# Performance work log

Hardware: AMD Instinct MI355X
Metric: run time of the kernel (lower is better)

## Reference

```python
import jax, jax.numpy as jnp
import numpy as np

N_ATOMS = 20
LS_PER_ATOM = [0, 0, 1, 1, 2]   # two s, two p, one d shell per atom
N_PRIM = 8
N_COORDS = 131072


def cart_angulars(l):
    return np.array([[lx, ly, l - lx - ly]
                     for lx in range(l, -1, -1)
                     for ly in range(l - lx, -1, -1)], dtype=np.float32)


def fact2(n):
    n = int(n)
    if n <= 0:
        return 1.0
    r = 1.0
    while n > 1:
        r *= n
        n -= 2
    return r


# ---- static shell bookkeeping (grouped by angular momentum l) ----
SHELL_ATOM = np.array([a for a in range(N_ATOMS) for _ in LS_PER_ATOM])
SHELL_L = np.array([l for _ in range(N_ATOMS) for l in LS_PER_ATOM])
N_SHELLS = len(SHELL_L)
UNIQUE_LS = sorted(set(LS_PER_ATOM))

GROUPS = {}
for l in UNIQUE_LS:
    idx = np.where(SHELL_L == l)[0]
    ls = cart_angulars(l)  # [ncart, 3]
    anorms = 1.0 / np.sqrt(np.array(
        [np.prod([fact2(2 * int(e) - 1) for e in row]) for row in ls],
        dtype=np.float64))
    GROUPS[l] = (idx, ls, anorms.astype(np.float32))

NAO_CART = sum(len(GROUPS[l][1]) * len(GROUPS[l][0]) for l in UNIQUE_LS)  # 280
NAO_SPH = sum((2 * l + 1) * len(GROUPS[l][0]) for l in UNIQUE_LS)          # 260


def setup_inputs() -> dict:
    key = jax.random.key(0)
    k1, k2, k3, k4, k5, k6 = jax.random.split(key, 6)
    coords = jax.random.normal(k1, (N_COORDS, 3), dtype=jnp.float32) * 2.0
    centers = jax.random.normal(k2, (N_ATOMS, 3), dtype=jnp.float32) * 3.0
    # Gaussian exponents must be positive
    zetas = jax.random.uniform(k3, (N_SHELLS, N_PRIM), dtype=jnp.float32,
                               minval=0.2, maxval=3.0)
    coeffs = jax.random.normal(k4, (N_SHELLS, N_PRIM), dtype=jnp.float32)
    normalization = jax.random.uniform(k5, (NAO_CART,), dtype=jnp.float32,
                                       minval=0.5, maxval=1.5)
    cart2sph = jax.random.normal(k6, (NAO_CART, NAO_SPH), dtype=jnp.float32) * 0.3
    return {"coords": coords, "centers": centers, "zetas": zetas,
            "coeffs": coeffs, "normalization": normalization,
            "cart2sph": cart2sph}


def reference(coords, centers, zetas, coeffs, normalization, cart2sph):
    """Batched GTOBasis.eval_ao: [N,3] -> [N, nao_sph]."""
    n = coords.shape[0]
    pieces = []
    for l in UNIQUE_LS:
        idx, ls, anorms = GROUPS[l]
        c = centers[SHELL_ATOM[idx]]                 # [S, 3]
        rs = coords[:, None, :] - c[None]            # [N, S, 3]
        rs2 = jnp.sum(rs * rs, axis=-1)              # [N, S]
        # cartesian angular part: prod over xyz of rs**l_component
        ang = jnp.prod(rs[:, :, None, :] ** jnp.asarray(ls)[None, None],
                       axis=-1)                      # [N, S, ncart]
        ex = jnp.exp(-zetas[idx][None] * rs2[:, :, None])  # [N, S, nprim]
        rad = jnp.sum(coeffs[idx][None] * ex, axis=-1)     # [N, S]
        phis = jnp.asarray(anorms) * ang * rad[:, :, None]  # [N, S, ncart]
        pieces.append(phis.reshape(n, -1))
    aos = jnp.concatenate(pieces, axis=-1) * normalization  # [N, nao_cart]
    return jnp.dot(aos, cart2sph)                           # [N, nao_sph]
```

## Files before the change

kernel.cpp:

```cpp
#include <hip/hip_runtime.h>

typedef unsigned int uint;
typedef unsigned short ushort;
typedef __attribute__((ext_vector_type(8))) short short8;
typedef __attribute__((ext_vector_type(4))) float f32x4;

#define NSH   100
#define NPRIM 8
#define NAOC  280
#define NAOS  260
#define NATOM 20
#define KP    288
#define NKB   9
#define MT    32
#define NTHR  256
#define NCOLP 272
#define BCH   (32 * NCOLP)
#define RSQRT3 0.57735026918962576f
#define LOG2E  1.4426950408889634f
#define EPS   276

#define O_AH    0
#define O_AL    18432
#define O_ZETA  36864
#define O_COEF  40064
#define O_CEN   43264
#define O_CX    43584
#define O_CY    43712
#define O_CZ    43840
#define POOLSZ  43968

__device__ __forceinline__ ushort bf16_rne(float x) {
    uint u = __float_as_uint(x);
    return (ushort)((u + 0x7FFFu + ((u >> 16) & 1u)) >> 16);
}
__device__ __forceinline__ float bf16_to_f(ushort h) {
    return __uint_as_float(((uint)h) << 16);
}
__device__ __forceinline__ uint cvt_pk_bf16(float a, float b) {
    uint r;
    asm("v_cvt_pk_bf16_f32 %0, %1, %2" : "=v"(r) : "v"(a), "v"(b));
    return r;
}

__device__ __forceinline__ float b_src(const float* __restrict__ c2s,
                                       const float* __restrict__ norm,
                                       int kp, int col) {
    if (kp >= NAOC || col >= NAOS) return 0.0f;
    int a = kp / 14, i = kp - 14 * a;
    int ksrc; float an = 1.0f;
    if (i < 2)      ksrc = 2 * a + i;
    else if (i < 8) ksrc = 40 + 6 * a + (i - 2);
    else {
        ksrc = 160 + 6 * a + (i - 8);
        if (i == 8 || i == 11 || i == 13) an = RSQRT3;
    }
    return c2s[ksrc * NAOS + col] * norm[ksrc] * an;
}

__global__ void prep_b(const float* __restrict__ c2s, const float* __restrict__ norm,
                       ushort* __restrict__ wsHi, ushort* __restrict__ wsLo) {
    int id = blockIdx.x * 256 + threadIdx.x;
    if (id >= KP * NCOLP) return;
    int k = id / NCOLP, col = id % NCOLP;
    float v = b_src(c2s, norm, k, col);
    ushort hi = bf16_rne(v);
    ushort lo = bf16_rne(v - bf16_to_f(hi));
    int off = (k >> 5) * BCH +
              (((col >> 4) * 4 + ((k & 31) >> 3)) * 16 + (col & 15)) * 8 + (k & 7);
    wsHi[off] = hi;
    wsLo[off] = lo;
}

template <bool USEWS>
__global__ __launch_bounds__(NTHR, 4) void gto_mfma(
    const float* __restrict__ coords, const float* __restrict__ centers,
    const float* __restrict__ zetas, const float* __restrict__ coeffs,
    const float* __restrict__ norm, const float* __restrict__ c2s,
    const ushort* __restrict__ wsHi, const ushort* __restrict__ wsLo,
    float* __restrict__ out, int n)
{
    __shared__ __align__(16) char smem[POOLSZ];
    float*  sZeta = (float*)(smem + O_ZETA);
    float*  sCoef = (float*)(smem + O_COEF);
    float4* sCen4 = (float4*)(smem + O_CEN);
    float*  sCx   = (float*)(smem + O_CX);
    float*  sCy   = (float*)(smem + O_CY);
    float*  sCz   = (float*)(smem + O_CZ);

    const int t = threadIdx.x, lane = t & 63, w = t >> 6;
    const int lr = lane & 15, lg4 = lane >> 4;
    const int P0 = blockIdx.x * MT;

    for (int i = t; i < NSH * NPRIM; i += NTHR) {
        sZeta[i] = zetas[i] * LOG2E;
        sCoef[i] = coeffs[i];
    }
    if (t < NATOM)
        sCen4[t] = make_float4(centers[3 * t], centers[3 * t + 1], centers[3 * t + 2], 0.0f);
    if (t < MT * 3) {
        int gi = P0 * 3 + t;
        float v = (gi < 3 * n) ? coords[gi] : 0.0f;
        int p = t / 3, c = t - 3 * (t / 3);
        if (c == 0) sCx[p] = v; else if (c == 1) sCy[p] = v; else sCz[p] = v;
    }
    if (t < 64)        *(uint2*)(smem + O_AH + 35 * 512 + t * 8) = make_uint2(0u, 0u);
    else if (t < 128)  *(uint2*)(smem + O_AL + 35 * 512 + (t - 64) * 8) = make_uint2(0u, 0u);
    __syncthreads();

    const int pA = t & 31, ag = t >> 5;
    const float cxp = sCx[pA], cyp = sCy[pA], czp = sCz[pA];

    auto doAtom = [&](int a) {
        float4 ca = sCen4[a];
        float dx = cxp - ca.x, dy = cyp - ca.y, dz = czp - ca.z;
        float r2 = dx * dx + dy * dy + dz * dz;
        float rad[5];
        #pragma unroll
        for (int sh = 0; sh < 5; ++sh) {
            const float* z = &sZeta[(5 * a + sh) * NPRIM];
            const float* cf = &sCoef[(5 * a + sh) * NPRIM];
            float4 z0 = *(const float4*)z,  z1 = *(const float4*)(z + 4);
            float4 c0 = *(const float4*)cf, c1 = *(const float4*)(cf + 4);
            float r = c0.x * __builtin_amdgcn_exp2f(-z0.x * r2);
            r += c0.y * __builtin_amdgcn_exp2f(-z0.y * r2);
            r += c0.z * __builtin_amdgcn_exp2f(-z0.z * r2);
            r += c0.w * __builtin_amdgcn_exp2f(-z0.w * r2);
            r += c1.x * __builtin_amdgcn_exp2f(-z1.x * r2);
            r += c1.y * __builtin_amdgcn_exp2f(-z1.y * r2);
            r += c1.z * __builtin_amdgcn_exp2f(-z1.z * r2);
            r += c1.w * __builtin_amdgcn_exp2f(-z1.w * r2);
            rad[sh] = r;
        }
        float xx = dx * dx, xy = dx * dy, xz = dx * dz;
        float yy = dy * dy, yz = dy * dz, zz = dz * dz;
        float v[14] = { rad[0], rad[1],
                        dx * rad[2], dy * rad[2], dz * rad[2],
                        dx * rad[3], dy * rad[3], dz * rad[3],
                        xx * rad[4], xy * rad[4], xz * rad[4],
                        yy * rad[4], yz * rad[4], zz * rad[4] };
        const int k0 = a * 14;
        #pragma unroll
        for (int pr = 0; pr < 7; ++pr) {
            int k = k0 + 2 * pr;
            uint h = cvt_pk_bf16(v[2 * pr], v[2 * pr + 1]);
            float r0 = v[2 * pr]     - __uint_as_float(h << 16);
            float r1 = v[2 * pr + 1] - __uint_as_float(h & 0xffff0000u);
            uint l = cvt_pk_bf16(r0, r1);
            const int off = (k >> 3) * 512 + pA * 16 + (k & 7) * 2;
            *(uint*)(smem + O_AH + off) = h;
            *(uint*)(smem + O_AL + off) = l;
        }
    };
    if (ag < 4) { doAtom(3 * ag); doAtom(3 * ag + 1); doAtom(3 * ag + 2); }
    else        { int b = 12 + 2 * (ag - 4); doAtom(b); doAtom(b + 1); }
    __syncthreads();

    const ushort* pH  = wsHi + (4 * w * 64 + lane) * 8;
    const ushort* pL  = wsLo + (4 * w * 64 + lane) * 8;
    const ushort* pH2 = wsHi + (16 * 64 + lane) * 8;
    const ushort* pL2 = wsLo + (16 * 64 + lane) * 8;

    f32x4 acc[5][2];
    #pragma unroll
    for (int i = 0; i < 5; ++i)
        #pragma unroll
        for (int mt = 0; mt < 2; ++mt)
            acc[i][mt] = (f32x4){0.0f, 0.0f, 0.0f, 0.0f};

    #pragma unroll 1
    for (int kb = 0; kb < NKB; ++kb) {
        short8 aH[2], aL[2];
        #pragma unroll
        for (int mt = 0; mt < 2; ++mt) {
            const int off = (kb * 4 + lg4) * 512 + (mt * 16 + lr) * 16;
            aH[mt] = *(const short8*)(smem + O_AH + off);
            aL[mt] = *(const short8*)(smem + O_AL + off);
        }
        #pragma unroll
        for (int i = 0; i < 5; ++i) {
            if (i < 4 || w == 0) {
                short8 bh, bl;
                if (USEWS) {
                    if (i < 4) { bh = *(const short8*)(pH + i * 512);
                                 bl = *(const short8*)(pL + i * 512); }
                    else       { bh = *(const short8*)pH2;
                                 bl = *(const short8*)pL2; }
                } else {
                    int nt = (i == 4) ? 16 : (4 * w + i);
                    #pragma unroll
                    for (int j = 0; j < 8; ++j) {
                        int k = kb * 32 + lg4 * 8 + j;
                        int col = nt * 16 + lr;
                        float v = b_src(c2s, norm, k, col);
                        ushort hi = bf16_rne(v);
                        bh[j] = (short)hi;
                        bl[j] = (short)bf16_rne(v - bf16_to_f(hi));
                    }
                }
                #pragma unroll
                for (int mt = 0; mt < 2; ++mt)
                    acc[i][mt] = __builtin_amdgcn_mfma_f32_16x16x32_bf16(aH[mt], bh, acc[i][mt], 0, 0, 0);
                #pragma unroll
                for (int mt = 0; mt < 2; ++mt)
                    acc[i][mt] = __builtin_amdgcn_mfma_f32_16x16x32_bf16(aH[mt], bl, acc[i][mt], 0, 0, 0);
                #pragma unroll
                for (int mt = 0; mt < 2; ++mt)
                    acc[i][mt] = __builtin_amdgcn_mfma_f32_16x16x32_bf16(aL[mt], bh, acc[i][mt], 0, 0, 0);
            }
        }
        pH += BCH; pL += BCH; pH2 += BCH; pL2 += BCH;
    }

    float* ep = (float*)smem;
    #pragma unroll
    for (int mt = 0; mt < 2; ++mt) {
        __syncthreads();
        #pragma unroll
        for (int i = 0; i < 5; ++i) {
            if (i < 4 || w == 0) {
                int nt = (i == 4) ? 16 : (4 * w + i);
                int col = nt * 16 + lr;
                #pragma unroll
                for (int r = 0; r < 4; ++r)
                    ep[(lg4 * 4 + r) * EPS + col] = acc[i][mt][r];
            }
        }
        __syncthreads();
        #pragma unroll
        for (int j = 0; j < 4; ++j) {
            int row = w + j * 4;
            int P = P0 + mt * 16 + row;
            if (P < n)
                *(float4*)&out[(size_t)P * NAOS + lane * 4] = *(const float4*)&ep[row * EPS + lane * 4];
        }
        if (w == 1 && lane < 16) {
            int P = P0 + mt * 16 + lane;
            if (P < n)
                *(float4*)&out[(size_t)P * NAOS + 256] = *(const float4*)&ep[lane * EPS + 256];
        }
    }
}

extern "C" void kernel_launch(void* const* d_in, const int* in_sizes, int n_in,
                              void* d_out, int out_size, void* d_ws, size_t ws_size,
                              hipStream_t stream) {
    const float* coords  = (const float*)d_in[0];
    const float* centers = (const float*)d_in[1];
    const float* zetas   = (const float*)d_in[2];
    const float* coeffs  = (const float*)d_in[3];
    const float* norm    = (const float*)d_in[4];
    const float* c2s     = (const float*)d_in[5];
    float* out = (float*)d_out;
    int n = in_sizes[0] / 3;
    int grid = (n + MT - 1) / MT;

    ushort* wsHi = (ushort*)d_ws;
    ushort* wsLo = wsHi + (size_t)KP * NCOLP;
    const size_t WS_NEED = (size_t)2 * KP * NCOLP * sizeof(ushort);

    if (ws_size >= WS_NEED) {
        prep_b<<<(KP * NCOLP + 255) / 256, 256, 0, stream>>>(c2s, norm, wsHi, wsLo);
        gto_mfma<true><<<grid, NTHR, 0, stream>>>(coords, centers, zetas, coeffs, norm, c2s,
                                                  wsHi, wsLo, out, n);
    } else {
        gto_mfma<false><<<grid, NTHR, 0, stream>>>(coords, centers, zetas, coeffs, norm, c2s,
                                                   nullptr, nullptr, out, n);
    }
}
```

Measured before the change: 91.88 us.

## Pad K to 16 per atom, vectorize A stores, hoist B loads, single epilogue

Repacks the K dimension so each atom occupies 16 slots (14 used, 2 zero), letting each atom's bf16 hi/lo values go to shared memory as 128-bit stores instead of many 32-bit stores, and drops the separate zero-fill of the padding. B fragments for all five N-tiles are loaded at the top of each K step so the global loads overlap instead of sitting between MFMAs. The epilogue writes both M-subtiles to shared memory in one pass with one barrier pair. The cost is an extra K block (10 instead of 9) of MFMA work, more shared memory, and occupancy lowered to 3 blocks per SM in the launch bounds.

```diff
diff --git a/kernel.cpp b/kernel.cpp
--- a/kernel.cpp
+++ b/kernel.cpp
@@ -10,8 +10,8 @@
 #define NAOC  280
 #define NAOS  260
 #define NATOM 20
-#define KP    288
-#define NKB   9
+#define KP    320
+#define NKB   10
 #define MT    32
 #define NTHR  256
 #define NCOLP 272
@@ -21,14 +21,14 @@
 #define EPS   276
 
 #define O_AH    0
-#define O_AL    18432
-#define O_ZETA  36864
-#define O_COEF  40064
-#define O_CEN   43264
-#define O_CX    43584
-#define O_CY    43712
-#define O_CZ    43840
-#define POOLSZ  43968
+#define O_AL    20480
+#define O_ZETA  40960
+#define O_COEF  44160
+#define O_CEN   47360
+#define O_CX    47680
+#define O_CY    47808
+#define O_CZ    47936
+#define POOLSZ  48064
 
 __device__ __forceinline__ ushort bf16_rne(float x) {
     uint u = __float_as_uint(x);
@@ -46,8 +46,9 @@
 __device__ __forceinline__ float b_src(const float* __restrict__ c2s,
                                        const float* __restrict__ norm,
                                        int kp, int col) {
-    if (kp >= NAOC || col >= NAOS) return 0.0f;
-    int a = kp / 14, i = kp - 14 * a;
+    if (kp >= KP || col >= NAOS) return 0.0f;
+    int a = kp >> 4, i = kp & 15;
+    if (i >= 14) return 0.0f;
     int ksrc; float an = 1.0f;
     if (i < 2)      ksrc = 2 * a + i;
     else if (i < 8) ksrc = 40 + 6 * a + (i - 2);
@@ -73,7 +74,7 @@
 }
 
 template <bool USEWS>
-__global__ __launch_bounds__(NTHR, 4) void gto_mfma(
+__global__ __launch_bounds__(NTHR, 3) void gto_mfma(
     const float* __restrict__ coords, const float* __restrict__ centers,
     const float* __restrict__ zetas, const float* __restrict__ coeffs,
     const float* __restrict__ norm, const float* __restrict__ c2s,
@@ -104,8 +105,6 @@
         int p = t / 3, c = t - 3 * (t / 3);
         if (c == 0) sCx[p] = v; else if (c == 1) sCy[p] = v; else sCz[p] = v;
     }
-    if (t < 64)        *(uint2*)(smem + O_AH + 35 * 512 + t * 8) = make_uint2(0u, 0u);
-    else if (t < 128)  *(uint2*)(smem + O_AL + 35 * 512 + (t - 64) * 8) = make_uint2(0u, 0u);
     __syncthreads();
 
     const int pA = t & 31, ag = t >> 5;
@@ -139,18 +138,19 @@
                         dx * rad[3], dy * rad[3], dz * rad[3],
                         xx * rad[4], xy * rad[4], xz * rad[4],
                         yy * rad[4], yz * rad[4], zz * rad[4] };
-        const int k0 = a * 14;
+        uint h[7], l[7];
         #pragma unroll
         for (int pr = 0; pr < 7; ++pr) {
-            int k = k0 + 2 * pr;
-            uint h = cvt_pk_bf16(v[2 * pr], v[2 * pr + 1]);
-            float r0 = v[2 * pr]     - __uint_as_float(h << 16);
-            float r1 = v[2 * pr + 1] - __uint_as_float(h & 0xffff0000u);
-            uint l = cvt_pk_bf16(r0, r1);
-            const int off = (k >> 3) * 512 + pA * 16 + (k & 7) * 2;
-            *(uint*)(smem + O_AH + off) = h;
-            *(uint*)(smem + O_AL + off) = l;
-        }
+            h[pr] = cvt_pk_bf16(v[2 * pr], v[2 * pr + 1]);
+            float r0 = v[2 * pr]     - __uint_as_float(h[pr] << 16);
+            float r1 = v[2 * pr + 1] - __uint_as_float(h[pr] & 0xffff0000u);
+            l[pr] = cvt_pk_bf16(r0, r1);
+        }
+        const int off = a * 1024 + pA * 16;
+        *(uint4*)(smem + O_AH + off)       = make_uint4(h[0], h[1], h[2], h[3]);
+        *(uint4*)(smem + O_AH + off + 512) = make_uint4(h[4], h[5], h[6], 0u);
+        *(uint4*)(smem + O_AL + off)       = make_uint4(l[0], l[1], l[2], l[3]);
+        *(uint4*)(smem + O_AL + off + 512) = make_uint4(l[4], l[5], l[6], 0u);
     };
     if (ag < 4) { doAtom(3 * ag); doAtom(3 * ag + 1); doAtom(3 * ag + 2); }
     else        { int b = 12 + 2 * (ag - 4); doAtom(b); doAtom(b + 1); }
@@ -170,6 +170,33 @@
 
     #pragma unroll 1
     for (int kb = 0; kb < NKB; ++kb) {
+        short8 bh[5], bl[5];
+        if (USEWS) {
+            #pragma unroll
+            for (int i = 0; i < 4; ++i) {
+                bh[i] = *(const short8*)(pH + i * 512);
+                bl[i] = *(const short8*)(pL + i * 512);
+            }
+            if (w == 0) {
+                bh[4] = *(const short8*)pH2;
+                bl[4] = *(const short8*)pL2;
+            }
+        } else {
+            #pragma unroll
+            for (int i = 0; i < 5; ++i) {
+                int nt = (i == 4) ? 16 : (4 * w + i);
+                #pragma unroll
+                for (int j = 0; j < 8; ++j) {
+                    int k = kb * 32 + lg4 * 8 + j;
+                    int col = nt * 16 + lr;
+                    float v = b_src(c2s, norm, k, col);
+                    ushort hi = bf16_rne(v);
+                    bh[i][j] = (short)hi;
+                    bl[i][j] = (short)bf16_rne(v - bf16_to_f(hi));
+                }
+            }
+        }
+
         short8 aH[2], aL[2];
         #pragma unroll
         for (int mt = 0; mt < 2; ++mt) {
@@ -177,68 +204,51 @@
             aH[mt] = *(const short8*)(smem + O_AH + off);
             aL[mt] = *(const short8*)(smem + O_AL + off);
         }
+
         #pragma unroll
         for (int i = 0; i < 5; ++i) {
             if (i < 4 || w == 0) {
-                short8 bh, bl;
-                if (USEWS) {
-                    if (i < 4) { bh = *(const short8*)(pH + i * 512);
-                                 bl = *(const short8*)(pL + i * 512); }
-                    else       { bh = *(const short8*)pH2;
-                                 bl = *(const short8*)pL2; }
-                } else {
-                    int nt = (i == 4) ? 16 : (4 * w + i);
-                    #pragma unroll
-                    for (int j = 0; j < 8; ++j) {
-                        int k = kb * 32 + lg4 * 8 + j;
-                        int col = nt * 16 + lr;
-                        float v = b_src(c2s, norm, k, col);
-                        ushort hi = bf16_rne(v);
-                        bh[j] = (short)hi;
-                        bl[j] = (short)bf16_rne(v - bf16_to_f(hi));
-                    }
-                }
                 #pragma unroll
                 for (int mt = 0; mt < 2; ++mt)
-                    acc[i][mt] = __builtin_amdgcn_mfma_f32_16x16x32_bf16(aH[mt], bh, acc[i][mt], 0, 0, 0);
+                    acc[i][mt] = __builtin_amdgcn_mfma_f32_16x16x32_bf16(aH[mt], bh[i], acc[i][mt], 0, 0, 0);
                 #pragma unroll
                 for (int mt = 0; mt < 2; ++mt)
-                    acc[i][mt] = __builtin_amdgcn_mfma_f32_16x16x32_bf16(aH[mt], bl, acc[i][mt], 0, 0, 0);
+                    acc[i][mt] = __builtin_amdgcn_mfma_f32_16x16x32_bf16(aH[mt], bl[i], acc[i][mt], 0, 0, 0);
                 #pragma unroll
                 for (int mt = 0; mt < 2; ++mt)
-                    acc[i][mt] = __builtin_amdgcn_mfma_f32_16x16x32_bf16(aL[mt], bh, acc[i][mt], 0, 0, 0);
+                    acc[i][mt] = __builtin_amdgcn_mfma_f32_16x16x32_bf16(aL[mt], bh[i], acc[i][mt], 0, 0, 0);
             }
         }
         pH += BCH; pL += BCH; pH2 += BCH; pL2 += BCH;
     }
 
+    __syncthreads();
     float* ep = (float*)smem;
     #pragma unroll
-    for (int mt = 0; mt < 2; ++mt) {
-        __syncthreads();
-        #pragma unroll
-        for (int i = 0; i < 5; ++i) {
-            if (i < 4 || w == 0) {
-                int nt = (i == 4) ? 16 : (4 * w + i);
-                int col = nt * 16 + lr;
+    for (int i = 0; i < 5; ++i) {
+        if (i < 4 || w == 0) {
+            int nt = (i == 4) ? 16 : (4 * w + i);
+            int col = nt * 16 + lr;
+            #pragma unroll
+            for (int mt = 0; mt < 2; ++mt)
                 #pragma unroll
                 for (int r = 0; r < 4; ++r)
-                    ep[(lg4 * 4 + r) * EPS + col] = acc[i][mt][r];
-            }
-        }
-        __syncthreads();
-        #pragma unroll
-        for (int j = 0; j < 4; ++j) {
-            int row = w + j * 4;
-            int P = P0 + mt * 16 + row;
-            if (P < n)
-                *(float4*)&out[(size_t)P * NAOS + lane * 4] = *(const float4*)&ep[row * EPS + lane * 4];
-        }
-        if (w == 1 && lane < 16) {
-            int P = P0 + mt * 16 + lane;
-            if (P < n)
-                *(float4*)&out[(size_t)P * NAOS + 256] = *(const float4*)&ep[lane * EPS + 256];
-        }
+                    ep[(mt * 16 + lg4 * 4 + r) * EPS + col] = acc[i][mt][r];
+        }
+    }
+    __syncthreads();
+
+    #pragma unroll
+    for (int j = 0; j < 8; ++j) {
+        int row = w + j * 4;
+        int P = P0 + row;
+        if (P < n)
+            *(float4*)&out[(size_t)P * NAOS + lane * 4] = *(const float4*)&ep[row * EPS + lane * 4];
+    }
+    if (w == 1 && lane < MT) {
+        int P = P0 + lane;
+        if (P < n)
+            *(float4*)&out[(size_t)P * NAOS + 256] = *(const float4*)&ep[lane * EPS + 256];
     }
 }
 
```

Result: faster. 89.71 us, median of 2 (-2.4%).
